# Optimization experiments

Measured on AMD Instinct MI355X. Metric: run time of the kernel, lower is better.

The kernel has to match this reference:

```python
import jax, jax.numpy as jnp
import numpy as np
from jax import lax

B, T_ENC, T_DEC, H, N_INP, OC = 1024, 48, 24, 128, 18, 0
F = N_INP - 1  # encoder1 input features (target column removed)


def _lstm_cell(x, h, c, Wih, Whh, bih, bhh):
    # PyTorch LSTMCell gate order: i, f, g, o
    g = x @ Wih.T + bih + h @ Whh.T + bhh
    i, f, gg, o = jnp.split(g, 4, axis=-1)
    c2 = jax.nn.sigmoid(f) * c + jax.nn.sigmoid(i) * jnp.tanh(gg)
    return jax.nn.sigmoid(o) * jnp.tanh(c2), c2


def setup_inputs() -> dict:
    key = jax.random.key(0)
    ks = jax.random.split(key, 32)
    w = lambda k, s: jax.random.normal(k, s, jnp.float32) * 0.05
    return {
        "input_p_q": jax.random.normal(ks[0], (B, T_ENC, N_INP), jnp.float32),
        "label_p": jax.random.normal(ks[1], (B, T_ENC), jnp.float32),
        "Ue1_W": w(ks[2], (T_ENC, T_ENC)), "Ue1_b": w(ks[3], (T_ENC,)),
        "We1_W": w(ks[4], (T_ENC, 2 * H)),
        "Ve1_W": w(ks[5], (1, T_ENC)), "Ve1_b": w(ks[6], (1,)),
        "Ue2_W": w(ks[7], (T_ENC, T_ENC)), "Ue2_b": w(ks[8], (T_ENC,)),
        "We2_W": w(ks[9], (T_ENC, 2 * H)),
        "Ve2_W": w(ks[10], (1, T_ENC)), "Ve2_b": w(ks[11], (1,)),
        "Ud_W": w(ks[12], (H, H)), "Ud_b": w(ks[13], (H,)),
        "Wd_W": w(ks[14], (H, 2 * H)),
        "Vd_W": w(ks[15], (1, H)), "Vd_b": w(ks[16], (1,)),
        "e1_Wih": w(ks[17], (4 * H, F)), "e1_Whh": w(ks[18], (4 * H, H)),
        "e1_bih": w(ks[19], (4 * H,)), "e1_bhh": w(ks[20], (4 * H,)),
        "e2_Wih": w(ks[21], (4 * H, H + 1)), "e2_Whh": w(ks[22], (4 * H, H)),
        "e2_bih": w(ks[23], (4 * H,)), "e2_bhh": w(ks[24], (4 * H,)),
        "d_Wih": w(ks[25], (4 * H, H)), "d_Whh": w(ks[26], (4 * H, H)),
        "d_bih": w(ks[27], (4 * H,)), "d_bhh": w(ks[28], (4 * H,)),
        "reg_W": w(ks[29], (1, H)), "reg_b": w(ks[30], (1,)),
    }


def reference(input_p_q, label_p, Ue1_W, Ue1_b, We1_W, Ve1_W, Ve1_b,
              Ue2_W, Ue2_b, We2_W, Ve2_W, Ve2_b, Ud_W, Ud_b, Wd_W, Vd_W, Vd_b,
              e1_Wih, e1_Whh, e1_bih, e1_bhh, e2_Wih, e2_Whh, e2_bih, e2_bhh,
              d_Wih, d_Whh, d_bih, d_bhh, reg_W, reg_b):
    b = input_p_q.shape[0]
    # drop the target column OC from the 18 input features
    x = jnp.concatenate([input_p_q[:, :T_ENC, :OC],
                         input_p_q[:, :T_ENC, OC + 1:N_INP]], axis=-1)  # [B,T,F]
    labels = label_p[:, :T_ENC]
    zeros = jnp.zeros((b, H), x.dtype)

    # ---- stage 1: spatial (input) attention + encoder1 LSTM ----
    pre1 = jnp.einsum('btf,st->bfs', x, Ue1_W) + Ue1_b  # Ue1(inputs^T), step-invariant: [B,F,T]

    def step1(carry, x_t):
        h, c = carry
        we = jnp.concatenate([h, c], axis=1) @ We1_W.T            # [B,T]
        e = jnp.tanh(we[:, None, :] + pre1)                        # [B,F,T]
        score = jnp.einsum('bft,t->bf', e, Ve1_W[0]) + Ve1_b[0]    # [B,F]
        h, c = _lstm_cell(x_t * jax.nn.softmax(score, axis=1), h, c,
                          e1_Wih, e1_Whh, e1_bih, e1_bhh)
        return (h, c), h

    _, mid = lax.scan(step1, (zeros, zeros), x.transpose(1, 0, 2))  # [T,B,H]
    mid = jnp.concatenate([mid.transpose(1, 0, 2), labels[:, :, None]], axis=2)  # [B,T,H+1]

    # ---- stage 2: second attention + encoder2 LSTM ----
    pre2 = jnp.einsum('btf,st->bfs', mid, Ue2_W) + Ue2_b  # [B,H+1,T]

    def step2(carry, m_t):
        h, c = carry
        we = jnp.concatenate([h, c], axis=1) @ We2_W.T            # [B,T]
        e = jnp.tanh(we[:, None, :] + pre2)                        # [B,H+1,T]
        score = jnp.einsum('bft,t->bf', e, Ve2_W[0]) + Ve2_b[0]    # [B,H+1]
        h, c = _lstm_cell(m_t * jax.nn.softmax(score, axis=1), h, c,
                          e2_Wih, e2_Whh, e2_bih, e2_bhh)
        return (h, c), h

    _, fin = lax.scan(step2, (zeros, zeros), mid.transpose(1, 0, 2))
    fin = fin.transpose(1, 0, 2)  # final_output: [B,T,H]

    # ---- decoder: temporal attention over final_output ----
    ud = fin @ Ud_W.T + Ud_b  # Ud(final_output), step-invariant: [B,T,H]

    def stepd(carry, _):
        hi, ci = carry
        wd = jnp.concatenate([hi, ci], axis=1) @ Wd_W.T            # [B,H]
        e = jnp.tanh(wd[:, None, :] + ud)                           # [B,T,H]
        score = jnp.einsum('bth,h->bt', e, Vd_W[0]) + Vd_b[0]       # [B,T]
        din = jnp.einsum('bt,bth->bh', jax.nn.softmax(score, axis=1), fin)
        hi, ci = _lstm_cell(din, hi, ci, d_Wih, d_Whh, d_bih, d_bhh)
        return (hi, ci), hi

    _, dec = lax.scan(stepd, (zeros, zeros), None, length=T_DEC + 6)  # [Td+6,B,H]
    out = dec.transpose(1, 0, 2) @ reg_W.T + reg_b                     # [B,Td+6,1]
    return out[:, -T_DEC:, 0]                                          # [B,T_DEC]
```

## Files before the change

### kernel.cpp

```cpp
#include <hip/hip_runtime.h>


#define T_ENC 48
#define H 128
#define FDIM 17
#define BBLK 2
#define NTH 512
#define GRID 512

#define H_WT1   0
#define H_WT2   77824
#define H_WTD   212992
#define H_WE1T  344064
#define H_WE2T  356352
#define H_WDT   368640
#define H_UDT   401408
#define F_B1    208896
#define F_B2    209408
#define F_BD    209920
#define F_MID   210432
#define F_FIN   6551040

typedef _Float16 h2_t __attribute__((ext_vector_type(2)));
union H2U { h2_t h; uint u; float f; };

__device__ __forceinline__ h2_t uh(uint v){ H2U x; x.u = v; return x.h; }
__device__ __forceinline__ h2_t fh(float v){ H2U x; x.f = v; return x.h; }
__device__ __forceinline__ uint pack2(float a, float b){
    H2U x; x.h[0] = (_Float16)a; x.h[1] = (_Float16)b; return x.u;
}
__device__ __forceinline__ float dot2f(h2_t a, h2_t b, float c){
#if __has_builtin(__builtin_amdgcn_fdot2)
    return __builtin_amdgcn_fdot2(a, b, c, false);
#else
    return c + (float)a[0]*(float)b[0] + (float)a[1]*(float)b[1];
#endif
}

__device__ __forceinline__ float fast_sigm(float x){
    return __fdividef(1.0f, 1.0f + __expf(-x));
}
__device__ __forceinline__ float fast_tanh(float x){
    float xc = fminf(fmaxf(x, -9.0f), 9.0f);
    float e = __expf(2.0f * xc);
    return __fdividef(e - 1.0f, e + 1.0f);
}

__global__ void prep_kernel(const float* __restrict__ We1W, const float* __restrict__ We2W,
                            const float* __restrict__ WdW,  const float* __restrict__ UdW,
                            const float* __restrict__ e1Wih, const float* __restrict__ e1Whh,
                            const float* __restrict__ e1bih, const float* __restrict__ e1bhh,
                            const float* __restrict__ e2Wih, const float* __restrict__ e2Whh,
                            const float* __restrict__ e2bih, const float* __restrict__ e2bhh,
                            const float* __restrict__ dWih,  const float* __restrict__ dWhh,
                            const float* __restrict__ dbih,  const float* __restrict__ dbhh,
                            float* __restrict__ ws)
{
    int idx = blockIdx.x * blockDim.x + threadIdx.x;
    _Float16* wsh = (_Float16*)ws;
    if (idx < 77824) {
        int k8 = idx >> 12, r = idx & 4095, j = r >> 3, kq = r & 7, k = k8*8 + kq;
        float v = 0.f;
        if (k < 17) v = e1Wih[j*17 + k]; else if (k < 145) v = e1Whh[j*128 + (k-17)];
        wsh[H_WT1 + idx] = (_Float16)v; return;
    }
    idx -= 77824;
    if (idx < 135168) {
        int k8 = idx >> 12, r = idx & 4095, j = r >> 3, kq = r & 7, k = k8*8 + kq;
        float v = 0.f;
        if (k < 129) v = e2Wih[j*129 + k]; else if (k < 257) v = e2Whh[j*128 + (k-129)];
        wsh[H_WT2 + idx] = (_Float16)v; return;
    }
    idx -= 135168;
    if (idx < 131072) {
        int k8 = idx >> 12, r = idx & 4095, j = r >> 3, kq = r & 7, k = k8*8 + kq;
        float v = (k < 128) ? dWih[j*128 + k] : dWhh[j*128 + (k-128)];
        wsh[H_WTD + idx] = (_Float16)v; return;
    }
    idx -= 131072;
    if (idx < 12288) {
        int pr = idx >> 1, p = idx & 1, k2 = pr / 48, s = pr % 48;
        wsh[H_WE1T + idx] = (_Float16)We1W[s*256 + 2*k2 + p]; return;
    }
    idx -= 12288;
    if (idx < 12288) {
        int pr = idx >> 1, p = idx & 1, k2 = pr / 48, s = pr % 48;
        wsh[H_WE2T + idx] = (_Float16)We2W[s*256 + 2*k2 + p]; return;
    }
    idx -= 12288;
    if (idx < 32768) {
        int pr = idx >> 1, p = idx & 1, k2 = pr >> 7, sp = pr & 127;
        wsh[H_WDT + idx] = (_Float16)WdW[sp*256 + 2*k2 + p]; return;
    }
    idx -= 32768;
    if (idx < 16384) {
        int pr = idx >> 1, p = idx & 1, k2 = pr >> 7, hh = pr & 127;
        wsh[H_UDT + idx] = (_Float16)UdW[hh*128 + 2*k2 + p]; return;
    }
    idx -= 16384;
    if (idx < 512) { ws[F_B1 + idx] = e1bih[idx] + e1bhh[idx]; return; }
    idx -= 512;
    if (idx < 512) { ws[F_B2 + idx] = e2bih[idx] + e2bhh[idx]; return; }
    idx -= 512;
    if (idx < 512) { ws[F_BD + idx] = dbih[idx] + dbhh[idx]; return; }
}

template<int K8>
__device__ __forceinline__ void lstm_gates2h(const float4* __restrict__ W8,
                                             const float* __restrict__ bias,
                                             const uint* u2, float* g, int tid)
{
    float a0 = bias[tid], a1 = a0;
    #pragma unroll 4
    for (int k8 = 0; k8 < K8; ++k8) {
        float4 w  = W8[k8*512 + tid];
        float4 ua = *(const float4*)(u2 + 4*k8);
        float4 ub = *(const float4*)(u2 + 132 + 4*k8);
        a0 = dot2f(fh(w.x), fh(ua.x), a0); a0 = dot2f(fh(w.y), fh(ua.y), a0);
        a0 = dot2f(fh(w.z), fh(ua.z), a0); a0 = dot2f(fh(w.w), fh(ua.w), a0);
        a1 = dot2f(fh(w.x), fh(ub.x), a1); a1 = dot2f(fh(w.y), fh(ub.y), a1);
        a1 = dot2f(fh(w.z), fh(ub.z), a1); a1 = dot2f(fh(w.w), fh(ub.w), a1);
    }
    g[tid] = a0; g[512 + tid] = a1;
}

__device__ __forceinline__ void softmax2(float* sc, float* at, int n, int tid)
{
    if (tid < 64) {
        int b = tid >> 5, i = tid & 31, base = b*129;
        float m = -1e30f;
        for (int f = i; f < n; f += 32) m = fmaxf(m, sc[base + f]);
        for (int o = 16; o; o >>= 1) m = fmaxf(m, __shfl_xor(m, o, 32));
        float ssum = 0.f;
        for (int f = i; f < n; f += 32) { float p = __expf(sc[base+f] - m); at[base+f] = p; ssum += p; }
        for (int o = 16; o; o >>= 1) ssum += __shfl_xor(ssum, o, 32);
        float inv = __fdividef(1.f, ssum);
        for (int f = i; f < n; f += 32) at[base + f] *= inv;
    }
}

__device__ __forceinline__ void we_phase_h(const uint* __restrict__ W2,
                                           const uint* h2, const uint* c2,
                                           float* sh_we, int tid)
{
    if (tid < 384) {
        int b = tid / 192, r = tid % 192, s = r >> 2, kq = r & 3;
        const uint* st2 = ((kq < 2) ? h2 : c2) + b*64 + (kq & 1)*32;
        const uint* w2  = W2 + (kq*32)*48 + s;
        float acc = 0.f;
        #pragma unroll 8
        for (int kk = 0; kk < 32; ++kk)
            acc = dot2f(uh(st2[kk]), uh(w2[kk*48]), acc);
        acc += __shfl_xor(acc, 1);
        acc += __shfl_xor(acc, 2);
        if (kq == 0) sh_we[b*48 + s] = acc;
    }
}

__global__ __launch_bounds__(NTH, 6)
void dstp_main(const float* __restrict__ ipq,  const float* __restrict__ labp,
               const float* __restrict__ Ue1W, const float* __restrict__ Ue1b,
               const float* __restrict__ Ve1,  const float* __restrict__ Ve1b,
               const float* __restrict__ Ue2W, const float* __restrict__ Ue2b,
               const float* __restrict__ Ve2,  const float* __restrict__ Ve2b,
               const float* __restrict__ Udb,
               const float* __restrict__ Vd,   const float* __restrict__ Vdb,
               const float* __restrict__ regW, const float* __restrict__ regb,
               float* __restrict__ ws, float* __restrict__ out)
{
    extern __shared__ float sm[];
    float* sh_h   = sm;
    float* sh_c   = sm + 256;
    float* sh_we  = sm + 512;
    float* sh_sc  = sm + 768;
    float* sh_at  = sm + 1028;
    float* sh_g   = sm + 1288;
    float* sh_x   = sm + 2312;
    float* sh_p1  = sm + 3944;
    uint*  sh_h2u = (uint*)(sm + 5576);
    uint*  sh_c2u = (uint*)(sm + 5704);
    uint*  sh_u2  = (uint*)(sm + 5832);
    _Float16* sh_bigh = (_Float16*)(sm + 6096);

    const int tid = threadIdx.x;
    const int b0  = blockIdx.x * BBLK;
    const _Float16* wsh = (const _Float16*)ws;

    for (int idx = tid; idx < BBLK*T_ENC*FDIM; idx += NTH) {
        int b = idx / (T_ENC*FDIM), r = idx % (T_ENC*FDIM), t = r / FDIM, f = r % FDIM;
        sh_x[idx] = ipq[((size_t)(b0 + b)*T_ENC + t)*18 + 1 + f];
    }
    if (tid < 256) { sh_h[tid] = 0.f; sh_c[tid] = 0.f; }
    if (tid < 128) { sh_h2u[tid] = 0u; sh_c2u[tid] = 0u; }
    if (tid < BBLK*T_ENC) {
        int b = tid / T_ENC, t = tid % T_ENC;
        ws[F_MID + ((size_t)(b0 + b)*T_ENC + t)*129 + 128] = labp[(size_t)(b0 + b)*T_ENC + t];
    }
    __syncthreads();
    for (int idx = tid; idx < BBLK*T_ENC*FDIM; idx += NTH) {
        int b = idx / (T_ENC*FDIM), r = idx % (T_ENC*FDIM), s = r / FDIM, f = r % FDIM;
        float acc = Ue1b[s];
        #pragma unroll 4
        for (int t = 0; t < T_ENC; ++t) acc = fmaf(sh_x[(b*T_ENC+t)*FDIM + f], Ue1W[s*T_ENC + t], acc);
        sh_p1[(b*T_ENC + s)*FDIM + f] = acc;
    }
    __syncthreads();

    const float ve1b = Ve1b[0];
    for (int t = 0; t < T_ENC; ++t) {
        we_phase_h((const uint*)(wsh + H_WE1T), sh_h2u, sh_c2u, sh_we, tid);
        __syncthreads();
        if (tid < 136) {
            int pair = tid >> 2, q = tid & 3, b = pair / FDIM, f = pair % FDIM;
            float acc = 0.f;
            for (int s = q; s < 48; s += 4)
                acc += fast_tanh(sh_we[b*48 + s] + sh_p1[(b*T_ENC + s)*FDIM + f]) * Ve1[s];
            acc += __shfl_xor(acc, 1);
            acc += __shfl_xor(acc, 2);
            if (q == 0) sh_sc[b*129 + f] = acc + ve1b;
        }
        __syncthreads();
        softmax2(sh_sc, sh_at, FDIM, tid);
        __syncthreads();
        if (tid < BBLK*152) {
            int b = tid / 152, kk = tid % 152;
            float v;
            if (kk < FDIM)        v = sh_x[(b*T_ENC + t)*FDIM + kk] * sh_at[b*129 + kk];
            else if (kk < FDIM+H) v = sh_h[b*H + (kk - FDIM)];
            else                  v = 0.f;
            float vnb = __shfl_xor(v, 1);
            if (!(tid & 1)) sh_u2[b*132 + (kk >> 1)] = pack2(v, vnb);
        }
        __syncthreads();
        lstm_gates2h<19>((const float4*)(wsh + H_WT1), ws + F_B1, sh_u2, sh_g, tid);
        __syncthreads();
        if (tid < 256) {
            int b = tid >> 7, jj = tid & 127;
            float gi = sh_g[b*512 + jj],       gf = sh_g[b*512 + 128 + jj];
            float gg = sh_g[b*512 + 256 + jj], go = sh_g[b*512 + 384 + jj];
            float c2v = fast_sigm(gf)*sh_c[tid] + fast_sigm(gi)*fast_tanh(gg);
            float hn  = fast_sigm(go)*fast_tanh(c2v);
            sh_c[tid] = c2v; sh_h[tid] = hn;
            ws[F_MID + ((size_t)(b0 + b)*T_ENC + t)*129 + jj] = hn;
            float hnb = __shfl_xor(hn, 1), cnb = __shfl_xor(c2v, 1);
            if (!(jj & 1)) {
                sh_h2u[b*64 + (jj >> 1)] = pack2(hn, hnb);
                sh_c2u[b*64 + (jj >> 1)] = pack2(c2v, cnb);
            }
        }
        __syncthreads();
    }

    for (int idx = tid; idx < BBLK*48*129; idx += NTH) {
        int b = idx / (48*129), r = idx % (48*129), s = r / 129, f = r % 129;
        const float* midb = ws + F_MID + (size_t)(b0 + b)*T_ENC*129 + f;
        float acc = Ue2b[s];
        #pragma unroll 4
        for (int t2 = 0; t2 < T_ENC; ++t2) acc = fmaf(midb[t2*129], Ue2W[s*48 + t2], acc);
        sh_bigh[(b*48 + s)*130 + f] = (_Float16)acc;
    }
    if (tid < 256) { sh_h[tid] = 0.f; sh_c[tid] = 0.f; }
    if (tid < 128) { sh_h2u[tid] = 0u; sh_c2u[tid] = 0u; }
    __syncthreads();

    const float ve2b = Ve2b[0];
    for (int t = 0; t < T_ENC; ++t) {
        we_phase_h((const uint*)(wsh + H_WE2T), sh_h2u, sh_c2u, sh_we, tid);
        __syncthreads();
        if (tid < 258) {
            int b = tid / 129, f = tid % 129;
            const _Float16* p2 = sh_bigh + b*48*130 + f;
            const float* wv = sh_we + b*48;
            float acc = 0.f;
            #pragma unroll 4
            for (int s = 0; s < 48; ++s)
                acc += fast_tanh(wv[s] + (float)p2[s*130]) * Ve2[s];
            sh_sc[b*129 + f] = acc + ve2b;
        }
        __syncthreads();
        softmax2(sh_sc, sh_at, 129, tid);
        __syncthreads();
        for (int idx = tid; idx < BBLK*264; idx += NTH) {
            int b = idx / 264, kk = idx % 264;
            const float* midrow = ws + F_MID + ((size_t)(b0 + b)*T_ENC + t)*129;
            float v;
            if (kk < 129)      v = midrow[kk] * sh_at[b*129 + kk];
            else if (kk < 257) v = sh_h[b*H + (kk - 129)];
            else               v = 0.f;
            float vnb = __shfl_xor(v, 1);
            if (!(idx & 1)) sh_u2[b*132 + ((kk) >> 1)] = pack2(v, vnb);
        }
        __syncthreads();
        lstm_gates2h<33>((const float4*)(wsh + H_WT2), ws + F_B2, sh_u2, sh_g, tid);
        __syncthreads();
        if (tid < 256) {
            int b = tid >> 7, jj = tid & 127;
            float gi = sh_g[b*512 + jj],       gf = sh_g[b*512 + 128 + jj];
            float gg = sh_g[b*512 + 256 + jj], go = sh_g[b*512 + 384 + jj];
            float c2v = fast_sigm(gf)*sh_c[tid] + fast_sigm(gi)*fast_tanh(gg);
            float hn  = fast_sigm(go)*fast_tanh(c2v);
            sh_c[tid] = c2v; sh_h[tid] = hn;
            ws[F_FIN + ((size_t)(b0 + b)*T_ENC + t)*128 + jj] = hn;
            float hnb = __shfl_xor(hn, 1), cnb = __shfl_xor(c2v, 1);
            if (!(jj & 1)) {
                sh_h2u[b*64 + (jj >> 1)] = pack2(hn, hnb);
                sh_c2u[b*64 + (jj >> 1)] = pack2(c2v, cnb);
            }
        }
        __syncthreads();
    }

    {
        uint* fin2 = (uint*)sh_bigh;
        const float4* fsrc = (const float4*)(ws + F_FIN + (size_t)b0*T_ENC*128);
        for (int idx = tid; idx < BBLK*T_ENC*32; idx += NTH) {
            float4 v = fsrc[idx];
            fin2[2*idx]     = pack2(v.x, v.y);
            fin2[2*idx + 1] = pack2(v.z, v.w);
        }
    }
    __syncthreads();
    {
        const int hh = tid & 127;
        const uint* UT2  = (const uint*)(wsh + H_UDT);
        const uint* fin2 = (const uint*)sh_bigh;
        float* uds = ws + F_MID + (size_t)b0*T_ENC*129;
        #pragma unroll
        for (int c = 0; c < 3; ++c) {
            float acc[8]; int rowb2[8];
            #pragma unroll
            for (int i = 0; i < 8; ++i) {
                int idx = (c*8 + i)*NTH + tid;
                int b = idx / 6144, r = idx % 6144, tt = r >> 7;
                rowb2[i] = (b*T_ENC + tt)*64;
                acc[i] = Udb[hh];
            }
            for (int k2 = 0; k2 < 64; ++k2) {
                h2_t w2 = uh(UT2[k2*128 + hh]);
                #pragma unroll
                for (int i = 0; i < 8; ++i) acc[i] = dot2f(uh(fin2[rowb2[i] + k2]), w2, acc[i]);
            }
            #pragma unroll
            for (int i = 0; i < 8; ++i) uds[(size_t)(c*8 + i)*NTH + tid] = acc[i];
        }
    }
    if (tid < 256) { sh_h[tid] = 0.f; sh_c[tid] = 0.f; }
    if (tid < 128) { sh_h2u[tid] = 0u; sh_c2u[tid] = 0u; }
    __syncthreads();
    {
        const float* uds = ws + F_MID + (size_t)b0*T_ENC*129;
        for (int idx = tid; idx < BBLK*T_ENC*128; idx += NTH) {
            int b = idx / 6144, r = idx % 6144, tt = r >> 7, h2i = r & 127;
            sh_bigh[(b*T_ENC + tt)*130 + h2i] = (_Float16)uds[idx];
        }
    }
    __syncthreads();

    const float vdb = Vdb[0], rb = regb[0];
    const float* fing = ws + F_FIN + (size_t)b0*T_ENC*128;
    for (int st = 0; st < 30; ++st) {
        {
            int b = tid >> 8, r = tid & 255, kh = r >> 7, sp = r & 127;
            const uint* st2 = (kh ? sh_c2u : sh_h2u) + b*64;
            const uint* W2  = (const uint*)(wsh + H_WDT) + (kh*64)*128 + sp;
            float acc = 0.f;
            #pragma unroll 8
            for (int kk = 0; kk < 64; ++kk)
                acc = dot2f(uh(st2[kk]), uh(W2[kk*128]), acc);
            sh_g[(b*2 + kh)*128 + sp] = acc;
        }
        __syncthreads();
        if (tid < 192) {
            int q = tid & 1, pair = tid >> 1, b = pair / 48, tt = pair % 48;
            const float* pg = sh_g + b*256;
            const _Float16* udrow = sh_bigh + (b*T_ENC + tt)*130;
            float acc = 0.f;
            int h0 = q*64;
            #pragma unroll 4
            for (int kk = 0; kk < 64; ++kk) {
                int hh = h0 + kk;
                float wd = pg[hh] + pg[128 + hh];
                acc += fast_tanh(wd + (float)udrow[hh]) * Vd[hh];
            }
            acc += __shfl_xor(acc, 1);
            if (q == 0) sh_sc[b*129 + tt] = acc + vdb;
        }
        __syncthreads();
        softmax2(sh_sc, sh_at, 48, tid);
        __syncthreads();
        if (tid < 256) {
            int b = tid >> 7, hh = tid & 127;
            const float* fb = fing + b*T_ENC*128 + hh;
            float acc = 0.f;
            #pragma unroll 4
            for (int tt = 0; tt < 48; ++tt) acc = fmaf(sh_at[b*129 + tt], fb[tt*128], acc);
            float anb = __shfl_xor(acc, 1);
            if (!(hh & 1)) sh_u2[b*132 + (hh >> 1)] = pack2(acc, anb);
        }
        if (tid < 128) {
            int b = tid >> 6, i = tid & 63;
            sh_u2[b*132 + 64 + i] = sh_h2u[b*64 + i];
        }
        __syncthreads();
        lstm_gates2h<32>((const float4*)(wsh + H_WTD), ws + F_BD, sh_u2, sh_g, tid);
        __syncthreads();
        if (tid < 256) {
            int b = tid >> 7, jj = tid & 127;
            float gi = sh_g[b*512 + jj],       gf = sh_g[b*512 + 128 + jj];
            float gg = sh_g[b*512 + 256 + jj], go = sh_g[b*512 + 384 + jj];
            float c2v = fast_sigm(gf)*sh_c[tid] + fast_sigm(gi)*fast_tanh(gg);
            float hn  = fast_sigm(go)*fast_tanh(c2v);
            sh_c[tid] = c2v; sh_h[tid] = hn;
            float hnb = __shfl_xor(hn, 1), cnb = __shfl_xor(c2v, 1);
            if (!(jj & 1)) {
                sh_h2u[b*64 + (jj >> 1)] = pack2(hn, hnb);
                sh_c2u[b*64 + (jj >> 1)] = pack2(c2v, cnb);
            }
        }
        __syncthreads();
        if (st >= 6 && tid < 128) {
            int b = tid >> 6, l = tid & 63;
            float v = sh_h[b*H + l]*regW[l] + sh_h[b*H + 64 + l]*regW[64 + l];
            for (int o = 32; o; o >>= 1) v += __shfl_xor(v, o);
            if (l == 0) out[(size_t)(b0 + b)*24 + (st - 6)] = v + rb;
        }
    }
}

extern "C" void kernel_launch(void* const* d_in, const int* in_sizes, int n_in,
                              void* d_out, int out_size, void* d_ws, size_t ws_size,
                              hipStream_t stream)
{
    const float* ipq   = (const float*)d_in[0];
    const float* labp  = (const float*)d_in[1];
    const float* Ue1W  = (const float*)d_in[2];
    const float* Ue1b  = (const float*)d_in[3];
    const float* We1W  = (const float*)d_in[4];
    const float* Ve1   = (const float*)d_in[5];
    const float* Ve1b  = (const float*)d_in[6];
    const float* Ue2W  = (const float*)d_in[7];
    const float* Ue2b  = (const float*)d_in[8];
    const float* We2W  = (const float*)d_in[9];
    const float* Ve2   = (const float*)d_in[10];
    const float* Ve2b  = (const float*)d_in[11];
    const float* UdW   = (const float*)d_in[12];
    const float* Udb   = (const float*)d_in[13];
    const float* WdW   = (const float*)d_in[14];
    const float* Vd    = (const float*)d_in[15];
    const float* Vdb   = (const float*)d_in[16];
    const float* e1Wih = (const float*)d_in[17];
    const float* e1Whh = (const float*)d_in[18];
    const float* e1bih = (const float*)d_in[19];
    const float* e1bhh = (const float*)d_in[20];
    const float* e2Wih = (const float*)d_in[21];
    const float* e2Whh = (const float*)d_in[22];
    const float* e2bih = (const float*)d_in[23];
    const float* e2bhh = (const float*)d_in[24];
    const float* dWih  = (const float*)d_in[25];
    const float* dWhh  = (const float*)d_in[26];
    const float* dbih  = (const float*)d_in[27];
    const float* dbhh  = (const float*)d_in[28];
    const float* regW  = (const float*)d_in[29];
    const float* regb  = (const float*)d_in[30];
    float* ws  = (float*)d_ws;
    float* out = (float*)d_out;

    prep_kernel<<<(417792 + 1536 + 255)/256, 256, 0, stream>>>(
        We1W, We2W, WdW, UdW,
        e1Wih, e1Whh, e1bih, e1bhh,
        e2Wih, e2Whh, e2bih, e2bhh,
        dWih, dWhh, dbih, dbhh, ws);

    const size_t smem = 12336u * sizeof(float);
    hipFuncSetAttribute((const void*)dstp_main,
                        hipFuncAttributeMaxDynamicSharedMemorySize, (int)smem);
    dstp_main<<<GRID, NTH, smem, stream>>>(
        ipq, labp, Ue1W, Ue1b, Ve1, Ve1b,
        Ue2W, Ue2b, Ve2, Ve2b,
        Udb, Vd, Vdb, regW, regb, ws, out);
}
```

Before: 1.814 ms.

## Process one batch element per block and keep final outputs in LDS

Switches from two batch rows per block to one, doubling the grid to 1024 blocks and splitting each dot product across more threads (split-K in the gate GEMV, the We phase and the attention reductions) to shorten the serial recurrence chain per block. The encoder-2 outputs are now stored as fp16 in shared memory instead of a global workspace, and the Ud projection is computed directly from LDS. This removes global round trips for the decoder inputs. The cost is that the LSTM weights are streamed once per batch element instead of being amortised over two rows, roughly doubling weight traffic from L2.

```diff
diff --git a/kernel.cpp b/kernel.cpp
--- a/kernel.cpp
+++ b/kernel.cpp
@@ -4,9 +4,8 @@
 #define T_ENC 48
 #define H 128
 #define FDIM 17
-#define BBLK 2
 #define NTH 512
-#define GRID 512
+#define GRID 1024
 
 #define H_WT1   0
 #define H_WT2   77824
@@ -19,7 +18,6 @@
 #define F_B2    209408
 #define F_BD    209920
 #define F_MID   210432
-#define F_FIN   6551040
 
 typedef _Float16 h2_t __attribute__((ext_vector_type(2)));
 union H2U { h2_t h; uint u; float f; };
@@ -106,58 +104,65 @@
 }
 
 template<int K8>
-__device__ __forceinline__ void lstm_gates2h(const float4* __restrict__ W8,
+__device__ __forceinline__ void lstm_gates1h(const float4* __restrict__ W8,
                                              const float* __restrict__ bias,
                                              const uint* u2, float* g, int tid)
 {
-    float a0 = bias[tid], a1 = a0;
-    #pragma unroll 4
-    for (int k8 = 0; k8 < K8; ++k8) {
-        float4 w  = W8[k8*512 + tid];
-        float4 ua = *(const float4*)(u2 + 4*k8);
-        float4 ub = *(const float4*)(u2 + 132 + 4*k8);
-        a0 = dot2f(fh(w.x), fh(ua.x), a0); a0 = dot2f(fh(w.y), fh(ua.y), a0);
-        a0 = dot2f(fh(w.z), fh(ua.z), a0); a0 = dot2f(fh(w.w), fh(ua.w), a0);
-        a1 = dot2f(fh(w.x), fh(ub.x), a1); a1 = dot2f(fh(w.y), fh(ub.y), a1);
-        a1 = dot2f(fh(w.z), fh(ub.z), a1); a1 = dot2f(fh(w.w), fh(ub.w), a1);
-    }
-    g[tid] = a0; g[512 + tid] = a1;
-}
-
-__device__ __forceinline__ void softmax2(float* sc, float* at, int n, int tid)
+    float a0 = bias[tid], a1 = 0.f;
+    #pragma unroll
+    for (int k8 = 0; k8 + 1 < K8; k8 += 2) {
+        float4 w0 = W8[k8*512 + tid];
+        float4 w1 = W8[(k8+1)*512 + tid];
+        float4 u0 = *(const float4*)(u2 + 4*k8);
+        float4 u1 = *(const float4*)(u2 + 4*k8 + 4);
+        a0 = dot2f(fh(w0.x), fh(u0.x), a0); a0 = dot2f(fh(w0.y), fh(u0.y), a0);
+        a0 = dot2f(fh(w0.z), fh(u0.z), a0); a0 = dot2f(fh(w0.w), fh(u0.w), a0);
+        a1 = dot2f(fh(w1.x), fh(u1.x), a1); a1 = dot2f(fh(w1.y), fh(u1.y), a1);
+        a1 = dot2f(fh(w1.z), fh(u1.z), a1); a1 = dot2f(fh(w1.w), fh(u1.w), a1);
+    }
+    if (K8 & 1) {
+        float4 w0 = W8[(K8-1)*512 + tid];
+        float4 u0 = *(const float4*)(u2 + 4*(K8-1));
+        a0 = dot2f(fh(w0.x), fh(u0.x), a0); a0 = dot2f(fh(w0.y), fh(u0.y), a0);
+        a0 = dot2f(fh(w0.z), fh(u0.z), a0); a0 = dot2f(fh(w0.w), fh(u0.w), a0);
+    }
+    g[tid] = a0 + a1;
+}
+
+__device__ __forceinline__ void softmax1(float* sc, float* at, int n, int tid)
 {
     if (tid < 64) {
-        int b = tid >> 5, i = tid & 31, base = b*129;
         float m = -1e30f;
-        for (int f = i; f < n; f += 32) m = fmaxf(m, sc[base + f]);
-        for (int o = 16; o; o >>= 1) m = fmaxf(m, __shfl_xor(m, o, 32));
+        for (int f = tid; f < n; f += 64) m = fmaxf(m, sc[f]);
+        for (int o = 32; o; o >>= 1) m = fmaxf(m, __shfl_xor(m, o));
         float ssum = 0.f;
-        for (int f = i; f < n; f += 32) { float p = __expf(sc[base+f] - m); at[base+f] = p; ssum += p; }
-        for (int o = 16; o; o >>= 1) ssum += __shfl_xor(ssum, o, 32);
+        for (int f = tid; f < n; f += 64) { float p = __expf(sc[f] - m); at[f] = p; ssum += p; }
+        for (int o = 32; o; o >>= 1) ssum += __shfl_xor(ssum, o);
         float inv = __fdividef(1.f, ssum);
-        for (int f = i; f < n; f += 32) at[base + f] *= inv;
-    }
-}
-
-__device__ __forceinline__ void we_phase_h(const uint* __restrict__ W2,
-                                           const uint* h2, const uint* c2,
-                                           float* sh_we, int tid)
+        for (int f = tid; f < n; f += 64) at[f] *= inv;
+    }
+}
+
+__device__ __forceinline__ void we_phase1(const uint* __restrict__ W2,
+                                          const uint* h2, const uint* c2,
+                                          float* sh_we, int tid)
 {
     if (tid < 384) {
-        int b = tid / 192, r = tid % 192, s = r >> 2, kq = r & 3;
-        const uint* st2 = ((kq < 2) ? h2 : c2) + b*64 + (kq & 1)*32;
-        const uint* w2  = W2 + (kq*32)*48 + s;
+        int s = tid >> 3, kq = tid & 7;
+        const uint* st2 = ((kq < 4) ? h2 : c2) + (kq & 3)*16;
+        const uint* w2  = W2 + (kq*16)*48 + s;
         float acc = 0.f;
-        #pragma unroll 8
-        for (int kk = 0; kk < 32; ++kk)
-            acc = dot2f(uh(st2[kk]), uh(w2[kk*48]), acc);
+        #pragma unroll
+        for (int i = 0; i < 16; ++i)
+            acc = dot2f(uh(st2[i]), uh(w2[i*48]), acc);
         acc += __shfl_xor(acc, 1);
         acc += __shfl_xor(acc, 2);
-        if (kq == 0) sh_we[b*48 + s] = acc;
-    }
-}
-
-__global__ __launch_bounds__(NTH, 6)
+        acc += __shfl_xor(acc, 4);
+        if (kq == 0) sh_we[s] = acc;
+    }
+}
+
+__global__ __launch_bounds__(NTH, 8)
 void dstp_main(const float* __restrict__ ipq,  const float* __restrict__ labp,
                const float* __restrict__ Ue1W, const float* __restrict__ Ue1b,
                const float* __restrict__ Ve1,  const float* __restrict__ Ve1b,
@@ -170,259 +175,231 @@
 {
     extern __shared__ float sm[];
     float* sh_h   = sm;
-    float* sh_c   = sm + 256;
-    float* sh_we  = sm + 512;
-    float* sh_sc  = sm + 768;
-    float* sh_at  = sm + 1028;
-    float* sh_g   = sm + 1288;
-    float* sh_x   = sm + 2312;
-    float* sh_p1  = sm + 3944;
-    uint*  sh_h2u = (uint*)(sm + 5576);
-    uint*  sh_c2u = (uint*)(sm + 5704);
-    uint*  sh_u2  = (uint*)(sm + 5832);
-    _Float16* sh_bigh = (_Float16*)(sm + 6096);
+    float* sh_c   = sm + 128;
+    float* sh_we  = sm + 256;
+    float* sh_sc  = sm + 320;
+    float* sh_sc2 = sm + 452;
+    float* sh_at  = sm + 584;
+    float* sh_g   = sm + 716;
+    float* sh_x   = sm + 1228;
+    float* sh_p1  = sm + 2044;
+    uint*  sh_h2u = (uint*)(sm + 2860);
+    uint*  sh_c2u = (uint*)(sm + 2924);
+    uint*  sh_u2  = (uint*)(sm + 2988);
+    _Float16* sh_p2h = (_Float16*)(sm + 3124);
+    _Float16* sh_fnh = (_Float16*)(sm + 6244);
+    uint*     sh_fn2 = (uint*)(sm + 6244);
 
     const int tid = threadIdx.x;
-    const int b0  = blockIdx.x * BBLK;
+    const int b0  = blockIdx.x;
     const _Float16* wsh = (const _Float16*)ws;
 
-    for (int idx = tid; idx < BBLK*T_ENC*FDIM; idx += NTH) {
-        int b = idx / (T_ENC*FDIM), r = idx % (T_ENC*FDIM), t = r / FDIM, f = r % FDIM;
-        sh_x[idx] = ipq[((size_t)(b0 + b)*T_ENC + t)*18 + 1 + f];
-    }
-    if (tid < 256) { sh_h[tid] = 0.f; sh_c[tid] = 0.f; }
-    if (tid < 128) { sh_h2u[tid] = 0u; sh_c2u[tid] = 0u; }
-    if (tid < BBLK*T_ENC) {
-        int b = tid / T_ENC, t = tid % T_ENC;
-        ws[F_MID + ((size_t)(b0 + b)*T_ENC + t)*129 + 128] = labp[(size_t)(b0 + b)*T_ENC + t];
-    }
+    for (int idx = tid; idx < T_ENC*FDIM; idx += NTH) {
+        int t = idx / FDIM, f = idx % FDIM;
+        sh_x[idx] = ipq[((size_t)b0*T_ENC + t)*18 + 1 + f];
+    }
+    if (tid < 128) { sh_h[tid] = 0.f; sh_c[tid] = 0.f; }
+    if (tid < 64)  { sh_h2u[tid] = 0u; sh_c2u[tid] = 0u; }
+    if (tid < T_ENC)
+        ws[F_MID + ((size_t)b0*T_ENC + tid)*129 + 128] = labp[(size_t)b0*T_ENC + tid];
     __syncthreads();
-    for (int idx = tid; idx < BBLK*T_ENC*FDIM; idx += NTH) {
-        int b = idx / (T_ENC*FDIM), r = idx % (T_ENC*FDIM), s = r / FDIM, f = r % FDIM;
+    for (int idx = tid; idx < T_ENC*FDIM; idx += NTH) {
+        int s = idx / FDIM, f = idx % FDIM;
         float acc = Ue1b[s];
         #pragma unroll 4
-        for (int t = 0; t < T_ENC; ++t) acc = fmaf(sh_x[(b*T_ENC+t)*FDIM + f], Ue1W[s*T_ENC + t], acc);
-        sh_p1[(b*T_ENC + s)*FDIM + f] = acc;
+        for (int t = 0; t < T_ENC; ++t) acc = fmaf(sh_x[t*FDIM + f], Ue1W[s*T_ENC + t], acc);
+        sh_p1[idx] = acc;
     }
     __syncthreads();
 
     const float ve1b = Ve1b[0];
     for (int t = 0; t < T_ENC; ++t) {
-        we_phase_h((const uint*)(wsh + H_WE1T), sh_h2u, sh_c2u, sh_we, tid);
-        __syncthreads();
-        if (tid < 136) {
-            int pair = tid >> 2, q = tid & 3, b = pair / FDIM, f = pair % FDIM;
+        we_phase1((const uint*)(wsh + H_WE1T), sh_h2u, sh_c2u, sh_we, tid);
+        __syncthreads();
+        if (tid < 68) {
+            int f = tid >> 2, q = tid & 3;
             float acc = 0.f;
             for (int s = q; s < 48; s += 4)
-                acc += fast_tanh(sh_we[b*48 + s] + sh_p1[(b*T_ENC + s)*FDIM + f]) * Ve1[s];
+                acc += fast_tanh(sh_we[s] + sh_p1[s*FDIM + f]) * Ve1[s];
             acc += __shfl_xor(acc, 1);
             acc += __shfl_xor(acc, 2);
-            if (q == 0) sh_sc[b*129 + f] = acc + ve1b;
-        }
-        __syncthreads();
-        softmax2(sh_sc, sh_at, FDIM, tid);
-        __syncthreads();
-        if (tid < BBLK*152) {
-            int b = tid / 152, kk = tid % 152;
+            if (q == 0) sh_sc[f] = acc + ve1b;
+        }
+        __syncthreads();
+        softmax1(sh_sc, sh_at, FDIM, tid);
+        __syncthreads();
+        if (tid < 152) {
+            int kk = tid;
             float v;
-            if (kk < FDIM)        v = sh_x[(b*T_ENC + t)*FDIM + kk] * sh_at[b*129 + kk];
-            else if (kk < FDIM+H) v = sh_h[b*H + (kk - FDIM)];
+            if (kk < FDIM)        v = sh_x[t*FDIM + kk] * sh_at[kk];
+            else if (kk < FDIM+H) v = sh_h[kk - FDIM];
             else                  v = 0.f;
             float vnb = __shfl_xor(v, 1);
-            if (!(tid & 1)) sh_u2[b*132 + (kk >> 1)] = pack2(v, vnb);
-        }
-        __syncthreads();
-        lstm_gates2h<19>((const float4*)(wsh + H_WT1), ws + F_B1, sh_u2, sh_g, tid);
-        __syncthreads();
-        if (tid < 256) {
-            int b = tid >> 7, jj = tid & 127;
-            float gi = sh_g[b*512 + jj],       gf = sh_g[b*512 + 128 + jj];
-            float gg = sh_g[b*512 + 256 + jj], go = sh_g[b*512 + 384 + jj];
-            float c2v = fast_sigm(gf)*sh_c[tid] + fast_sigm(gi)*fast_tanh(gg);
+            if (!(kk & 1)) sh_u2[kk >> 1] = pack2(v, vnb);
+        }
+        __syncthreads();
+        lstm_gates1h<19>((const float4*)(wsh + H_WT1), ws + F_B1, sh_u2, sh_g, tid);
+        __syncthreads();
+        if (tid < 128) {
+            int jj = tid;
+            float gi = sh_g[jj],       gf = sh_g[128 + jj];
+            float gg = sh_g[256 + jj], go = sh_g[384 + jj];
+            float c2v = fast_sigm(gf)*sh_c[jj] + fast_sigm(gi)*fast_tanh(gg);
             float hn  = fast_sigm(go)*fast_tanh(c2v);
-            sh_c[tid] = c2v; sh_h[tid] = hn;
-            ws[F_MID + ((size_t)(b0 + b)*T_ENC + t)*129 + jj] = hn;
+            sh_c[jj] = c2v; sh_h[jj] = hn;
+            ws[F_MID + ((size_t)b0*T_ENC + t)*129 + jj] = hn;
             float hnb = __shfl_xor(hn, 1), cnb = __shfl_xor(c2v, 1);
             if (!(jj & 1)) {
-                sh_h2u[b*64 + (jj >> 1)] = pack2(hn, hnb);
-                sh_c2u[b*64 + (jj >> 1)] = pack2(c2v, cnb);
+                sh_h2u[jj >> 1] = pack2(hn, hnb);
+                sh_c2u[jj >> 1] = pack2(c2v, cnb);
             }
         }
         __syncthreads();
     }
 
-    for (int idx = tid; idx < BBLK*48*129; idx += NTH) {
-        int b = idx / (48*129), r = idx % (48*129), s = r / 129, f = r % 129;
-        const float* midb = ws + F_MID + (size_t)(b0 + b)*T_ENC*129 + f;
+    for (int idx = tid; idx < 48*129; idx += NTH) {
+        int s = idx / 129, f = idx % 129;
+        const float* midb = ws + F_MID + (size_t)b0*T_ENC*129 + f;
         float acc = Ue2b[s];
         #pragma unroll 4
         for (int t2 = 0; t2 < T_ENC; ++t2) acc = fmaf(midb[t2*129], Ue2W[s*48 + t2], acc);
-        sh_bigh[(b*48 + s)*130 + f] = (_Float16)acc;
-    }
-    if (tid < 256) { sh_h[tid] = 0.f; sh_c[tid] = 0.f; }
-    if (tid < 128) { sh_h2u[tid] = 0u; sh_c2u[tid] = 0u; }
+        sh_p2h[s*130 + f] = (_Float16)acc;
+    }
+    if (tid < 128) { sh_h[tid] = 0.f; sh_c[tid] = 0.f; }
+    if (tid < 64)  { sh_h2u[tid] = 0u; sh_c2u[tid] = 0u; }
     __syncthreads();
 
     const float ve2b = Ve2b[0];
     for (int t = 0; t < T_ENC; ++t) {
-        we_phase_h((const uint*)(wsh + H_WE2T), sh_h2u, sh_c2u, sh_we, tid);
+        we_phase1((const uint*)(wsh + H_WE2T), sh_h2u, sh_c2u, sh_we, tid);
         __syncthreads();
         if (tid < 258) {
-            int b = tid / 129, f = tid % 129;
-            const _Float16* p2 = sh_bigh + b*48*130 + f;
-            const float* wv = sh_we + b*48;
+            int f = (tid < 129) ? tid : tid - 129;
+            int s0 = (tid < 129) ? 0 : 24;
+            const _Float16* p2 = sh_p2h + f;
             float acc = 0.f;
             #pragma unroll 4
-            for (int s = 0; s < 48; ++s)
-                acc += fast_tanh(wv[s] + (float)p2[s*130]) * Ve2[s];
-            sh_sc[b*129 + f] = acc + ve2b;
-        }
-        __syncthreads();
-        softmax2(sh_sc, sh_at, 129, tid);
-        __syncthreads();
-        for (int idx = tid; idx < BBLK*264; idx += NTH) {
-            int b = idx / 264, kk = idx % 264;
-            const float* midrow = ws + F_MID + ((size_t)(b0 + b)*T_ENC + t)*129;
+            for (int s = s0; s < s0 + 24; ++s)
+                acc += fast_tanh(sh_we[s] + (float)p2[s*130]) * Ve2[s];
+            ((tid < 129) ? sh_sc : sh_sc2)[f] = acc;
+        }
+        __syncthreads();
+        if (tid < 129) sh_sc[tid] = sh_sc[tid] + sh_sc2[tid] + ve2b;
+        __syncthreads();
+        softmax1(sh_sc, sh_at, 129, tid);
+        __syncthreads();
+        if (tid < 264) {
+            int kk = tid;
+            const float* midrow = ws + F_MID + ((size_t)b0*T_ENC + t)*129;
             float v;
-            if (kk < 129)      v = midrow[kk] * sh_at[b*129 + kk];
-            else if (kk < 257) v = sh_h[b*H + (kk - 129)];
+            if (kk < 129)      v = midrow[kk] * sh_at[kk];
+            else if (kk < 257) v = sh_h[kk - 129];
             else               v = 0.f;
             float vnb = __shfl_xor(v, 1);
-            if (!(idx & 1)) sh_u2[b*132 + ((kk) >> 1)] = pack2(v, vnb);
-        }
-        __syncthreads();
-        lstm_gates2h<33>((const float4*)(wsh + H_WT2), ws + F_B2, sh_u2, sh_g, tid);
-        __syncthreads();
-        if (tid < 256) {
-            int b = tid >> 7, jj = tid & 127;
-            float gi = sh_g[b*512 + jj],       gf = sh_g[b*512 + 128 + jj];
-            float gg = sh_g[b*512 + 256 + jj], go = sh_g[b*512 + 384 + jj];
-            float c2v = fast_sigm(gf)*sh_c[tid] + fast_sigm(gi)*fast_tanh(gg);
+            if (!(kk & 1)) sh_u2[kk >> 1] = pack2(v, vnb);
+        }
+        __syncthreads();
+        lstm_gates1h<33>((const float4*)(wsh + H_WT2), ws + F_B2, sh_u2, sh_g, tid);
+        __syncthreads();
+        if (tid < 128) {
+            int jj = tid;
+            float gi = sh_g[jj],       gf = sh_g[128 + jj];
+            float gg = sh_g[256 + jj], go = sh_g[384 + jj];
+            float c2v = fast_sigm(gf)*sh_c[jj] + fast_sigm(gi)*fast_tanh(gg);
             float hn  = fast_sigm(go)*fast_tanh(c2v);
-            sh_c[tid] = c2v; sh_h[tid] = hn;
-            ws[F_FIN + ((size_t)(b0 + b)*T_ENC + t)*128 + jj] = hn;
+            sh_c[jj] = c2v; sh_h[jj] = hn;
+            sh_fnh[t*128 + jj] = (_Float16)hn;
             float hnb = __shfl_xor(hn, 1), cnb = __shfl_xor(c2v, 1);
             if (!(jj & 1)) {
-                sh_h2u[b*64 + (jj >> 1)] = pack2(hn, hnb);
-                sh_c2u[b*64 + (jj >> 1)] = pack2(c2v, cnb);
+                sh_h2u[jj >> 1] = pack2(hn, hnb);
+                sh_c2u[jj >> 1] = pack2(c2v, cnb);
             }
         }
         __syncthreads();
     }
 
     {
-        uint* fin2 = (uint*)sh_bigh;
-        const float4* fsrc = (const float4*)(ws + F_FIN + (size_t)b0*T_ENC*128);
-        for (int idx = tid; idx < BBLK*T_ENC*32; idx += NTH) {
-            float4 v = fsrc[idx];
-            fin2[2*idx]     = pack2(v.x, v.y);
-            fin2[2*idx + 1] = pack2(v.z, v.w);
-        }
-    }
+        int hh = tid & 127, tg = tid >> 7;
+        float acc[12];
+        float ub = Udb[hh];
+        #pragma unroll
+        for (int i = 0; i < 12; ++i) acc[i] = ub;
+        const uint* UT2 = (const uint*)(wsh + H_UDT);
+        for (int k2 = 0; k2 < 64; ++k2) {
+            h2_t w2 = uh(UT2[k2*128 + hh]);
+            #pragma unroll
+            for (int i = 0; i < 12; ++i)
+                acc[i] = dot2f(uh(sh_fn2[(tg + 4*i)*64 + k2]), w2, acc[i]);
+        }
+        #pragma unroll
+        for (int i = 0; i < 12; ++i)
+            sh_p2h[(tg + 4*i)*130 + hh] = (_Float16)acc[i];
+    }
+    if (tid < 128) { sh_h[tid] = 0.f; sh_c[tid] = 0.f; }
+    if (tid < 64)  { sh_h2u[tid] = 0u; sh_c2u[tid] = 0u; }
     __syncthreads();
-    {
-        const int hh = tid & 127;
-        const uint* UT2  = (const uint*)(wsh + H_UDT);
-        const uint* fin2 = (const uint*)sh_bigh;
-        float* uds = ws + F_MID + (size_t)b0*T_ENC*129;
-        #pragma unroll
-        for (int c = 0; c < 3; ++c) {
-            float acc[8]; int rowb2[8];
-            #pragma unroll
-            for (int i = 0; i < 8; ++i) {
-                int idx = (c*8 + i)*NTH + tid;
-                int b = idx / 6144, r = idx % 6144, tt = r >> 7;
-                rowb2[i] = (b*T_ENC + tt)*64;
-                acc[i] = Udb[hh];
-            }
-            for (int k2 = 0; k2 < 64; ++k2) {
-                h2_t w2 = uh(UT2[k2*128 + hh]);
-                #pragma unroll
-                for (int i = 0; i < 8; ++i) acc[i] = dot2f(uh(fin2[rowb2[i] + k2]), w2, acc[i]);
-            }
-            #pragma unroll
-            for (int i = 0; i < 8; ++i) uds[(size_t)(c*8 + i)*NTH + tid] = acc[i];
-        }
-    }
-    if (tid < 256) { sh_h[tid] = 0.f; sh_c[tid] = 0.f; }
-    if (tid < 128) { sh_h2u[tid] = 0u; sh_c2u[tid] = 0u; }
-    __syncthreads();
-    {
-        const float* uds = ws + F_MID + (size_t)b0*T_ENC*129;
-        for (int idx = tid; idx < BBLK*T_ENC*128; idx += NTH) {
-            int b = idx / 6144, r = idx % 6144, tt = r >> 7, h2i = r & 127;
-            sh_bigh[(b*T_ENC + tt)*130 + h2i] = (_Float16)uds[idx];
-        }
-    }
-    __syncthreads();
 
     const float vdb = Vdb[0], rb = regb[0];
-    const float* fing = ws + F_FIN + (size_t)b0*T_ENC*128;
     for (int st = 0; st < 30; ++st) {
         {
-            int b = tid >> 8, r = tid & 255, kh = r >> 7, sp = r & 127;
-            const uint* st2 = (kh ? sh_c2u : sh_h2u) + b*64;
-            const uint* W2  = (const uint*)(wsh + H_WDT) + (kh*64)*128 + sp;
+            int kq = tid >> 7, sp = tid & 127;
+            const uint* st2 = ((kq < 2) ? sh_h2u : sh_c2u) + (kq & 1)*32;
+            const uint* W2  = (const uint*)(wsh + H_WDT) + (kq*32)*128 + sp;
             float acc = 0.f;
             #pragma unroll 8
-            for (int kk = 0; kk < 64; ++kk)
-                acc = dot2f(uh(st2[kk]), uh(W2[kk*128]), acc);
-            sh_g[(b*2 + kh)*128 + sp] = acc;
+            for (int i = 0; i < 32; ++i)
+                acc = dot2f(uh(st2[i]), uh(W2[i*128]), acc);
+            sh_g[kq*128 + sp] = acc;
         }
         __syncthreads();
         if (tid < 192) {
-            int q = tid & 1, pair = tid >> 1, b = pair / 48, tt = pair % 48;
-            const float* pg = sh_g + b*256;
-            const _Float16* udrow = sh_bigh + (b*T_ENC + tt)*130;
+            int tt = tid >> 2, q = tid & 3, h0 = q*32;
+            const _Float16* udrow = sh_p2h + tt*130;
             float acc = 0.f;
-            int h0 = q*64;
             #pragma unroll 4
-            for (int kk = 0; kk < 64; ++kk) {
+            for (int kk = 0; kk < 32; ++kk) {
                 int hh = h0 + kk;
-                float wd = pg[hh] + pg[128 + hh];
+                float wd = sh_g[hh] + sh_g[128 + hh] + sh_g[256 + hh] + sh_g[384 + hh];
                 acc += fast_tanh(wd + (float)udrow[hh]) * Vd[hh];
             }
             acc += __shfl_xor(acc, 1);
-            if (q == 0) sh_sc[b*129 + tt] = acc + vdb;
-        }
-        __syncthreads();
-        softmax2(sh_sc, sh_at, 48, tid);
+            acc += __shfl_xor(acc, 2);
+            if (q == 0) sh_sc[tt] = acc + vdb;
+        }
+        __syncthreads();
+        softmax1(sh_sc, sh_at, 48, tid);
         __syncthreads();
         if (tid < 256) {
-            int b = tid >> 7, hh = tid & 127;
-            const float* fb = fing + b*T_ENC*128 + hh;
+            int q = tid & 1, hh = tid >> 1;
             float acc = 0.f;
-            #pragma unroll 4
-            for (int tt = 0; tt < 48; ++tt) acc = fmaf(sh_at[b*129 + tt], fb[tt*128], acc);
-            float anb = __shfl_xor(acc, 1);
-            if (!(hh & 1)) sh_u2[b*132 + (hh >> 1)] = pack2(acc, anb);
-        }
+            for (int tt = q; tt < 48; tt += 2)
+                acc = fmaf(sh_at[tt], (float)sh_fnh[tt*128 + hh], acc);
+            acc += __shfl_xor(acc, 1);
+            float anb = __shfl_xor(acc, 2);
+            if (!(tid & 3)) sh_u2[tid >> 2] = pack2(acc, anb);
+        }
+        if (tid < 64) sh_u2[64 + tid] = sh_h2u[tid];
+        __syncthreads();
+        lstm_gates1h<32>((const float4*)(wsh + H_WTD), ws + F_BD, sh_u2, sh_g, tid);
+        __syncthreads();
         if (tid < 128) {
-            int b = tid >> 6, i = tid & 63;
-            sh_u2[b*132 + 64 + i] = sh_h2u[b*64 + i];
-        }
-        __syncthreads();
-        lstm_gates2h<32>((const float4*)(wsh + H_WTD), ws + F_BD, sh_u2, sh_g, tid);
-        __syncthreads();
-        if (tid < 256) {
-            int b = tid >> 7, jj = tid & 127;
-            float gi = sh_g[b*512 + jj],       gf = sh_g[b*512 + 128 + jj];
-            float gg = sh_g[b*512 + 256 + jj], go = sh_g[b*512 + 384 + jj];
-            float c2v = fast_sigm(gf)*sh_c[tid] + fast_sigm(gi)*fast_tanh(gg);
+            int jj = tid;
+            float gi = sh_g[jj],       gf = sh_g[128 + jj];
+            float gg = sh_g[256 + jj], go = sh_g[384 + jj];
+            float c2v = fast_sigm(gf)*sh_c[jj] + fast_sigm(gi)*fast_tanh(gg);
             float hn  = fast_sigm(go)*fast_tanh(c2v);
-            sh_c[tid] = c2v; sh_h[tid] = hn;
+            sh_c[jj] = c2v; sh_h[jj] = hn;
             float hnb = __shfl_xor(hn, 1), cnb = __shfl_xor(c2v, 1);
             if (!(jj & 1)) {
-                sh_h2u[b*64 + (jj >> 1)] = pack2(hn, hnb);
-                sh_c2u[b*64 + (jj >> 1)] = pack2(c2v, cnb);
+                sh_h2u[jj >> 1] = pack2(hn, hnb);
+                sh_c2u[jj >> 1] = pack2(c2v, cnb);
             }
         }
         __syncthreads();
-        if (st >= 6 && tid < 128) {
-            int b = tid >> 6, l = tid & 63;
-            float v = sh_h[b*H + l]*regW[l] + sh_h[b*H + 64 + l]*regW[64 + l];
+        if (st >= 6 && tid < 64) {
+            float v = sh_h[tid]*regW[tid] + sh_h[64 + tid]*regW[64 + tid];
             for (int o = 32; o; o >>= 1) v += __shfl_xor(v, o);
-            if (l == 0) out[(size_t)(b0 + b)*24 + (st - 6)] = v + rb;
+            if (tid == 0) out[(size_t)b0*24 + (st - 6)] = v + rb;
         }
     }
 }
@@ -471,7 +448,7 @@
         e2Wih, e2Whh, e2bih, e2bhh,
         dWih, dWhh, dbih, dbhh, ws);
 
-    const size_t smem = 12336u * sizeof(float);
+    const size_t smem = 9316u * sizeof(float);
     hipFuncSetAttribute((const void*)dstp_main,
                         hipFuncAttributeMaxDynamicSharedMemorySize, (int)smem);
     dstp_main<<<GRID, NTH, smem, stream>>>(
```

Measured after the change: 2.855 ms. 1.57x slower.
